# Kernel tuning notes

Hardware: AMD Instinct MI355X
Metric: run time of the kernel (lower is better)

The kernel has to match this reference:

```python
import jax, jax.numpy as jnp
import numpy as np
import math

B, T, D = 2, 2048, 1024
H = 16
DH = D // H  # 64
ROPE_BASE = 10000.0


def _rope_tables(seq_len, d_head, dtype=jnp.float32):
    inv_freq = 1.0 / (ROPE_BASE ** (jnp.arange(0, d_head, 2, dtype=jnp.float32) / d_head))
    pos = jnp.arange(seq_len, dtype=jnp.float32)
    freqs = jnp.outer(pos, inv_freq)            # [T, DH/2]
    emb = jnp.concatenate([freqs, freqs], -1)   # [T, DH]
    return jnp.cos(emb).astype(dtype), jnp.sin(emb).astype(dtype)


def _rotate_half(x):
    half = x.shape[-1] // 2
    return jnp.concatenate([-x[..., half:], x[..., :half]], axis=-1)


def setup_inputs() -> dict:
    key = jax.random.key(0)
    k1, k2, k3 = jax.random.split(key, 3)
    x = jax.random.normal(k1, (B, T, D), dtype=jnp.float32)
    qkv_w = jax.random.normal(k2, (D, 3 * D), dtype=jnp.float32) * (1.0 / math.sqrt(D))
    out_w = jax.random.normal(k3, (D, D), dtype=jnp.float32) * (1.0 / math.sqrt(D))
    out_b = jnp.zeros((D,), dtype=jnp.float32)
    mask = jnp.tril(jnp.ones((T, T), dtype=bool))[None, None]  # causal [1,1,T,T]
    return {"x": x, "mask": mask, "qkv_w": qkv_w, "out_w": out_w, "out_b": out_b}


def reference(x, mask, qkv_w, out_w, out_b):
    Bv, Tv, Dv = x.shape
    qkv = (x @ qkv_w).reshape(Bv, Tv, 3, H, DH)
    # [B, H, T, DH]
    q = jnp.transpose(qkv[:, :, 0], (0, 2, 1, 3))
    k = jnp.transpose(qkv[:, :, 1], (0, 2, 1, 3))
    v = jnp.transpose(qkv[:, :, 2], (0, 2, 1, 3))
    cos, sin = _rope_tables(Tv, DH, x.dtype)
    cos = cos[None, None]  # [1,1,T,DH]
    sin = sin[None, None]
    q = q * cos + _rotate_half(q) * sin
    k = k * cos + _rotate_half(k) * sin
    scores = jnp.einsum('bhqd,bhkd->bhqk', q, k) / math.sqrt(DH)
    scores = jnp.where(mask, scores, -jnp.inf)
    probs = jax.nn.softmax(scores, axis=-1)  # dropout = identity in eval mode
    out = jnp.einsum('bhqk,bhkd->bhqd', probs, v)
    out = jnp.transpose(out, (0, 2, 1, 3)).reshape(Bv, Tv, Dv)
    return out @ out_w + out_b
```

## Files before the change

kernel.cpp:

```cpp
#include <hip/hip_runtime.h>
#include <math.h>

typedef __attribute__((ext_vector_type(8))) short short8;
typedef __attribute__((ext_vector_type(4))) float f32x4;

static __device__ __forceinline__ unsigned short f2bf(float f) {
  unsigned u = __builtin_bit_cast(unsigned, f);
  u += 0x7fffu + ((u >> 16) & 1u);
  return (unsigned short)(u >> 16);
}
static __device__ __forceinline__ float bf2f(unsigned short h) {
  return __builtin_bit_cast(float, ((unsigned)h) << 16);
}
static __device__ __forceinline__ unsigned pack2bf(float a, float b) {
  return (unsigned)f2bf(a) | ((unsigned)f2bf(b) << 16);
}
static __device__ __forceinline__ unsigned pack2bf_t(float a, float b) {
  return __builtin_amdgcn_perm(__builtin_bit_cast(unsigned, b),
                               __builtin_bit_cast(unsigned, a), 0x07060302u);
}

typedef __attribute__((address_space(3))) unsigned short lds_us;
typedef __attribute__((address_space(1))) const unsigned short gbl_us;

static __device__ __forceinline__ void gld_lds16(const unsigned short* g,
                                                 unsigned short* l) {
  __builtin_amdgcn_global_load_lds((gbl_us*)g, (lds_us*)l, 16, 0, 0);
}

__global__ __launch_bounds__(256) void cast_x(const float* __restrict__ x,
                                              unsigned short* __restrict__ xb) {
  int i = (blockIdx.x * 256 + threadIdx.x) * 8;
  float4 a = *(const float4*)(x + i);
  float4 b = *(const float4*)(x + i + 4);
  ushort4 u0 = {f2bf(a.x), f2bf(a.y), f2bf(a.z), f2bf(a.w)};
  ushort4 u1 = {f2bf(b.x), f2bf(b.y), f2bf(b.z), f2bf(b.w)};
  *(ushort4*)(xb + i) = u0;
  *(ushort4*)(xb + i + 4) = u1;
}

__global__ __launch_bounds__(256) void tcast(const float* __restrict__ in,
                                             unsigned short* __restrict__ out,
                                             int R, int C) {
  __shared__ unsigned short T[64][68];
  const int r0 = blockIdx.y * 64, c0 = blockIdx.x * 64;
  const int tr = threadIdx.x >> 2;
  const int tc = (threadIdx.x & 3) * 16;
#pragma unroll
  for (int j = 0; j < 4; ++j) {
    float4 v = *(const float4*)(in + (size_t)(r0 + tr) * C + c0 + tc + j * 4);
    ushort4 u = {f2bf(v.x), f2bf(v.y), f2bf(v.z), f2bf(v.w)};
    *(ushort4*)&T[tr][tc + j * 4] = u;
  }
  __syncthreads();
  const int oc = tr;
#pragma unroll
  for (int g = 0; g < 4; ++g) {
    ushort4 u;
    u.x = T[tc + g * 4 + 0][oc];
    u.y = T[tc + g * 4 + 1][oc];
    u.z = T[tc + g * 4 + 2][oc];
    u.w = T[tc + g * 4 + 3][oc];
    *(ushort4*)(out + (size_t)(c0 + oc) * R + r0 + tc + g * 4) = u;
  }
}

template <int MODE>
__global__ __launch_bounds__(256) void gemm_mfma(
    const unsigned short* __restrict__ A, const unsigned short* __restrict__ BT,
    unsigned short* __restrict__ qo, unsigned short* __restrict__ ko,
    unsigned short* __restrict__ vo, const float* __restrict__ bias,
    float* __restrict__ out) {
  __shared__ unsigned short As[4096];
  __shared__ unsigned short Bs[4096];
  const int tid = threadIdx.x;
  const int w = tid >> 6;
  const int lane = tid & 63;
  const int l15 = lane & 15;
  const int quad = lane >> 4;
  const int wm = w >> 1, wn = w & 1;
  const int m0 = blockIdx.y * 128;
  const int n0 = blockIdx.x * 128;

  f32x4 acc[4][4];
  const f32x4 zero4 = {0.f, 0.f, 0.f, 0.f};
#pragma unroll
  for (int mt = 0; mt < 4; ++mt)
#pragma unroll
    for (int nt = 0; nt < 4; ++nt) acc[mt][nt] = zero4;

  int srow[2], skch[2];
#pragma unroll
  for (int i = 0; i < 2; ++i) {
    int c = i * 256 + w * 64 + lane;
    srow[i] = c >> 2;
    skch[i] = (c & 3) ^ ((srow[i] >> 1) & 3);
  }
  const unsigned short* gA[2];
  const unsigned short* gB[2];
#pragma unroll
  for (int i = 0; i < 2; ++i) {
    gA[i] = A + (size_t)(m0 + srow[i]) * 1024 + skch[i] * 8;
    gB[i] = BT + (size_t)(n0 + srow[i]) * 1024 + skch[i] * 8;
  }
  unsigned short* lA[2];
  unsigned short* lB[2];
#pragma unroll
  for (int i = 0; i < 2; ++i) {
    int c = i * 256 + w * 64 + lane;
    lA[i] = As + c * 8;
    lB[i] = Bs + c * 8;
  }

  const int swz = (quad ^ ((l15 >> 1) & 3)) * 8;
  int aoff[4], boff[4];
#pragma unroll
  for (int t = 0; t < 4; ++t) {
    aoff[t] = (wm * 64 + t * 16 + l15) * 32 + swz;
    boff[t] = (wn * 64 + t * 16 + l15) * 32 + swz;
  }

  for (int k0 = 0; k0 < 1024; k0 += 32) {
    __syncthreads();
#pragma unroll
    for (int i = 0; i < 2; ++i) {
      gld_lds16(gA[i] + k0, lA[i]);
      gld_lds16(gB[i] + k0, lB[i]);
    }
    __syncthreads();

    short8 af[4], bf[4];
#pragma unroll
    for (int t = 0; t < 4; ++t) {
      af[t] = *(const short8*)(As + aoff[t]);
      bf[t] = *(const short8*)(Bs + boff[t]);
    }
#pragma unroll
    for (int mt = 0; mt < 4; ++mt)
#pragma unroll
      for (int nt = 0; nt < 4; ++nt)
        acc[mt][nt] =
            __builtin_amdgcn_mfma_f32_16x16x32_bf16(af[mt], bf[nt], acc[mt][nt], 0, 0, 0);
  }

  if constexpr (MODE == 0) {
    const int b = m0 >> 11;
    const int nbase = n0 + wn * 64;
    const int which = nbase >> 10;
    const int h = (nbase & 1023) >> 6;
    const int bh = b * 16 + h;
    if (which < 2) {
      unsigned short* dst = which ? ko : qo;
      const float qs = (which == 0) ? 0.1803368801111f : 1.0f;
      float inv0 = expf(-((float)l15 / 32.f) * 9.21034037198f);
      float inv1 = expf(-((float)(16 + l15) / 32.f) * 9.21034037198f);
#pragma unroll
      for (int mt = 0; mt < 4; ++mt)
#pragma unroll
        for (int r = 0; r < 4; ++r) {
          int t = (m0 + wm * 64 + mt * 16 + quad * 4 + r) & 2047;
          float s0, c0, s1, c1;
          sincosf((float)t * inv0, &s0, &c0);
          sincosf((float)t * inv1, &s1, &c1);
          float x0 = acc[mt][0][r], x1 = acc[mt][1][r];
          float x2 = acc[mt][2][r], x3 = acc[mt][3][r];
          size_t rowoff = ((size_t)bh * 2048 + t) * 64 + l15;
          dst[rowoff + 0]  = f2bf((x0 * c0 - x2 * s0) * qs);
          dst[rowoff + 16] = f2bf((x1 * c1 - x3 * s1) * qs);
          dst[rowoff + 32] = f2bf((x2 * c0 + x0 * s0) * qs);
          dst[rowoff + 48] = f2bf((x3 * c1 + x1 * s1) * qs);
        }
    } else {
#pragma unroll
      for (int mt = 0; mt < 4; ++mt) {
        int t0 = (m0 + wm * 64 + mt * 16 + quad * 4) & 2047;
#pragma unroll
        for (int nt = 0; nt < 4; ++nt) {
          int dh = nt * 16 + l15;
          ushort4 st = {f2bf(acc[mt][nt][0]), f2bf(acc[mt][nt][1]),
                        f2bf(acc[mt][nt][2]), f2bf(acc[mt][nt][3])};
          *(ushort4*)(vo + ((size_t)bh * 64 + dh) * 2048 + t0) = st;
        }
      }
    }
  } else {
    const int nbase = n0 + wn * 64;
    float bv[4];
#pragma unroll
    for (int nt = 0; nt < 4; ++nt) bv[nt] = bias[nbase + nt * 16 + l15];
#pragma unroll
    for (int mt = 0; mt < 4; ++mt)
#pragma unroll
      for (int r = 0; r < 4; ++r) {
        int m = m0 + wm * 64 + mt * 16 + quad * 4 + r;
        float* orow = out + (size_t)m * 1024 + nbase + l15;
#pragma unroll
        for (int nt = 0; nt < 4; ++nt) orow[nt * 16] = acc[mt][nt][r] + bv[nt];
      }
  }
}

__global__ __launch_bounds__(256) void attn_mfma(
    const unsigned short* __restrict__ qg, const unsigned short* __restrict__ kg,
    const unsigned short* __restrict__ vtg, unsigned short* __restrict__ og,
    unsigned short* __restrict__ OpA,
    unsigned short* __restrict__ OpB,
    float* __restrict__ Lpart) {
  __shared__ unsigned short Ks[2][4096];
  __shared__ unsigned short Vt[2][4096];
  __shared__ unsigned short Ps[4 * 16 * 64];
  const int bh = blockIdx.y;
  const int slot = blockIdx.x;
  int qb, chunk;
  if (slot < 32) {
    qb = 24 + (slot & 7);
    chunk = slot >> 3;
  } else if (slot < 56) {
    int s = slot - 32;
    qb = 16 + (s & 7);
    chunk = s >> 3;
  } else if (slot < 72) {
    int s = slot - 56;
    qb = 8 + (s & 7);
    chunk = s >> 3;
  } else {
    qb = slot - 72;
    chunk = 0;
  }
  const int n = qb >= 24 ? 4 : (qb >= 16 ? 3 : (qb >= 8 ? 2 : 1));
  const int t0 = chunk * (qb + 1) / n;
  const int t1 = (chunk + 1) * (qb + 1) / n;

  const int tid = threadIdx.x;
  const int w = tid >> 6;
  const int lane = tid & 63;
  const int l15 = lane & 15;
  const int quad = lane >> 4;

  const int gq0 = qb * 64;
  const int qw = w * 16;

  const unsigned short* qrow = qg + ((size_t)bh * 2048 + gq0 + qw + l15) * 64;
  short8 qf0 = *(const short8*)(qrow + quad * 8);
  short8 qf1 = *(const short8*)(qrow + quad * 8 + 32);

  f32x4 acc_o[4];
  const f32x4 zero4 = {0.f, 0.f, 0.f, 0.f};
#pragma unroll
  for (int nt = 0; nt < 4; ++nt) acc_o[nt] = zero4;
  float lsum = 0.f;

  const unsigned short* kbase = kg + (size_t)bh * 2048 * 64;
  const unsigned short* vtbase = vtg + (size_t)bh * 64 * 2048;
  unsigned short* pb = &Ps[w * 16 * 64];
  const int prow = l15 * 64;
  const int psw = l15 & 7;

  auto issue = [&](int kb, int buf) {
    const unsigned short* ksrc = kbase + (size_t)(kb * 64) * 64;
    const unsigned short* vsrc = vtbase + kb * 64;
#pragma unroll
    for (int i = 0; i < 2; ++i) {
      int c = (w * 2 + i) * 64 + lane;
      int row = c >> 3, d = c & 7;
      int sc = d ^ (row & 7);
      gld_lds16(ksrc + row * 64 + sc * 8, &Ks[buf][c * 8]);
      gld_lds16(vsrc + (size_t)row * 2048 + sc * 8, &Vt[buf][c * 8]);
    }
  };

  const int kc0 = (quad ^ psw) * 8;
  const int kc1 = kc0 ^ 32;

  issue(t0, 0);
  for (int kb = t0; kb < t1; ++kb) {
    const int cur = (kb - t0) & 1;
    __syncthreads();
    if (kb + 1 < t1) issue(kb + 1, cur ^ 1);

    const unsigned short* kt = Ks[cur];
    const unsigned short* vt = Vt[cur];

    f32x4 s[4];
#pragma unroll
    for (int nt = 0; nt < 4; ++nt) {
      const unsigned short* kr = kt + (nt * 16 + l15) * 64;
      short8 kf0 = *(const short8*)(kr + kc0);
      short8 kf1 = *(const short8*)(kr + kc1);
      f32x4 c = zero4;
      c = __builtin_amdgcn_mfma_f32_16x16x32_bf16(kf0, qf0, c, 0, 0, 0);
      c = __builtin_amdgcn_mfma_f32_16x16x32_bf16(kf1, qf1, c, 0, 0, 0);
      s[nt] = c;
    }

    if (kb == qb) {
#pragma unroll
      for (int nt = 0; nt < 4; ++nt) {
        int klocal = nt * 16 + quad * 4;
        int qlocal = qw + l15;
#pragma unroll
        for (int r = 0; r < 4; ++r)
          if (klocal + r > qlocal) s[nt][r] = -INFINITY;
      }
    }

#pragma unroll
    for (int nt = 0; nt < 4; ++nt) {
      float e0 = exp2f(s[nt][0]);
      float e1 = exp2f(s[nt][1]);
      float e2 = exp2f(s[nt][2]);
      float e3 = exp2f(s[nt][3]);
      lsum += (e0 + e1) + (e2 + e3);
      int base = prow + ((nt * 2 + (quad >> 1)) ^ psw) * 8 + (quad & 1) * 4;
      *(unsigned*)&pb[base] = pack2bf_t(e0, e1);
      *(unsigned*)&pb[base + 2] = pack2bf_t(e2, e3);
    }

    short8 pf0 = *(const short8*)&pb[prow + (quad ^ psw) * 8];
    short8 pf1 = *(const short8*)&pb[prow + ((4 + quad) ^ psw) * 8];

#pragma unroll
    for (int nt = 0; nt < 4; ++nt) {
      const unsigned short* vr = vt + (nt * 16 + l15) * 64;
      short8 vf0 = *(const short8*)(vr + kc0);
      short8 vf1 = *(const short8*)(vr + kc1);
      acc_o[nt] = __builtin_amdgcn_mfma_f32_16x16x32_bf16(vf0, pf0, acc_o[nt], 0, 0, 0);
      acc_o[nt] = __builtin_amdgcn_mfma_f32_16x16x32_bf16(vf1, pf1, acc_o[nt], 0, 0, 0);
    }
  }

  lsum += __shfl_xor(lsum, 16);
  lsum += __shfl_xor(lsum, 32);

  if (n == 1) {
    float inv_l = 1.0f / lsum;
    const int b = bh >> 4;
    const int h = bh & 15;
    unsigned short* orow =
        og + ((size_t)(b * 2048 + gq0 + qw + l15)) * 1024 + h * 64 + quad * 4;
#pragma unroll
    for (int nt = 0; nt < 4; ++nt) {
      *(unsigned*)(orow + nt * 16) =
          pack2bf(acc_o[nt][0] * inv_l, acc_o[nt][1] * inv_l);
      *(unsigned*)(orow + nt * 16 + 2) =
          pack2bf(acc_o[nt][2] * inv_l, acc_o[nt][3] * inv_l);
    }
  } else {
    const int pidx = (qb < 16) ? (qb - 8) * 2 + chunk
                               : (qb < 24) ? 16 + (qb - 16) * 3 + chunk
                                           : 40 + (qb - 24) * 4 + chunk;
    unsigned short* obase = (pidx < 16)
                                ? OpB + ((size_t)(bh * 16 + pidx)) * 4096
                                : OpA + ((size_t)(bh * 56 + (pidx - 16))) * 4096;
    unsigned short* orow = obase + (qw + l15) * 64 + quad * 4;
#pragma unroll
    for (int nt = 0; nt < 4; ++nt) {
      *(unsigned*)(orow + nt * 16) = pack2bf(acc_o[nt][0], acc_o[nt][1]);
      *(unsigned*)(orow + nt * 16 + 2) = pack2bf(acc_o[nt][2], acc_o[nt][3]);
    }
    if (quad == 0) Lpart[(bh * 72 + pidx) * 64 + qw + l15] = lsum;
  }
}

__global__ __launch_bounds__(256) void attn_combine(
    const unsigned short* __restrict__ OpA, const unsigned short* __restrict__ OpB,
    const float* __restrict__ Lpart, unsigned short* __restrict__ og) {
  int i = blockIdx.x * 256 + threadIdx.x;
  int dh = (i & 15) * 4;
  int q = (i >> 4) & 63;
  int idx = i >> 10;
  int bh = idx / 24;
  int qr = idx - bh * 24;
  int qb = 8 + qr;
  int count = qr < 8 ? 2 : (qr < 16 ? 3 : 4);
  int pstart = qr < 8 ? qr * 2 : (qr < 16 ? 16 + (qr - 8) * 3 : 40 + (qr - 16) * 4);
  float o0 = 0.f, o1 = 0.f, o2 = 0.f, o3 = 0.f, l = 0.f;
  for (int c = 0; c < count; ++c) {
    int pidx = pstart + c;
    const unsigned short* obase =
        (pidx < 16) ? OpB + ((size_t)(bh * 16 + pidx)) * 4096
                    : OpA + ((size_t)(bh * 56 + (pidx - 16))) * 4096;
    ushort4 a = *(const ushort4*)(obase + q * 64 + dh);
    o0 += bf2f(a.x);
    o1 += bf2f(a.y);
    o2 += bf2f(a.z);
    o3 += bf2f(a.w);
    l += Lpart[(bh * 72 + pidx) * 64 + q];
  }
  float inv = 1.0f / l;
  int bb = bh >> 4, h = bh & 15;
  int t = qb * 64 + q;
  unsigned short* orow = og + ((size_t)(bb * 2048 + t)) * 1024 + h * 64 + dh;
  *(unsigned*)(orow) = pack2bf(o0 * inv, o1 * inv);
  *(unsigned*)(orow + 2) = pack2bf(o2 * inv, o3 * inv);
}

extern "C" void kernel_launch(void* const* d_in, const int* in_sizes, int n_in,
                              void* d_out, int out_size, void* d_ws,
                              size_t ws_size, hipStream_t stream) {
  const float* x = (const float*)d_in[0];
  const float* qkv_w = (const float*)d_in[2];
  const float* out_w = (const float*)d_in[3];
  const float* out_b = (const float*)d_in[4];
  float* out = (float*)d_out;

  unsigned short* xb = (unsigned short*)d_ws;
  unsigned short* wqkvT = xb + 4194304;
  unsigned short* woT = wqkvT + 3145728;
  unsigned short* qb16 = woT + 1048576;
  unsigned short* kb16 = qb16 + 4194304;
  unsigned short* vt16 = kb16 + 4194304;
  unsigned short* ab = vt16 + 4194304;
  unsigned short* OpB = ab + 4194304;
  float* Lpart = (float*)(OpB + 4194304);
  unsigned short* OpA = xb;

  cast_x<<<2048, 256, 0, stream>>>(x, xb);
  tcast<<<dim3(48, 16), 256, 0, stream>>>(qkv_w, wqkvT, 1024, 3072);
  tcast<<<dim3(16, 16), 256, 0, stream>>>(out_w, woT, 1024, 1024);
  gemm_mfma<0><<<dim3(24, 32), 256, 0, stream>>>(xb, wqkvT, qb16, kb16, vt16,
                                                 nullptr, nullptr);
  attn_mfma<<<dim3(80, 32), 256, 0, stream>>>(qb16, kb16, vt16, ab, OpA, OpB,
                                              Lpart);
  attn_combine<<<3072, 256, 0, stream>>>(OpA, OpB, Lpart, ab);
  gemm_mfma<1><<<dim3(8, 32), 256, 0, stream>>>(ab, woT, nullptr, nullptr,
                                                nullptr, out_b, out);
}
```

Before: 217.6 us.

## Double-buffer LDS tiles in MFMA GEMM to overlap loads with compute

```diff
diff --git a/kernel.cpp b/kernel.cpp
--- a/kernel.cpp
+++ b/kernel.cpp
@@ -71,8 +71,8 @@
     unsigned short* __restrict__ qo, unsigned short* __restrict__ ko,
     unsigned short* __restrict__ vo, const float* __restrict__ bias,
     float* __restrict__ out) {
-  __shared__ unsigned short As[4096];
-  __shared__ unsigned short Bs[4096];
+  __shared__ unsigned short As[2][4096];
+  __shared__ unsigned short Bs[2][4096];
   const int tid = threadIdx.x;
   const int w = tid >> 6;
   const int lane = tid & 63;
@@ -89,27 +89,17 @@
 #pragma unroll
     for (int nt = 0; nt < 4; ++nt) acc[mt][nt] = zero4;
 
-  int srow[2], skch[2];
+  int coff[2];
+  const unsigned short* gA[2];
+  const unsigned short* gB[2];
 #pragma unroll
   for (int i = 0; i < 2; ++i) {
     int c = i * 256 + w * 64 + lane;
-    srow[i] = c >> 2;
-    skch[i] = (c & 3) ^ ((srow[i] >> 1) & 3);
-  }
-  const unsigned short* gA[2];
-  const unsigned short* gB[2];
-#pragma unroll
-  for (int i = 0; i < 2; ++i) {
-    gA[i] = A + (size_t)(m0 + srow[i]) * 1024 + skch[i] * 8;
-    gB[i] = BT + (size_t)(n0 + srow[i]) * 1024 + skch[i] * 8;
-  }
-  unsigned short* lA[2];
-  unsigned short* lB[2];
-#pragma unroll
-  for (int i = 0; i < 2; ++i) {
-    int c = i * 256 + w * 64 + lane;
-    lA[i] = As + c * 8;
-    lB[i] = Bs + c * 8;
+    int srow = c >> 2;
+    int skch = (c & 3) ^ ((srow >> 1) & 3);
+    coff[i] = c * 8;
+    gA[i] = A + (size_t)(m0 + srow) * 1024 + skch * 8;
+    gB[i] = BT + (size_t)(n0 + srow) * 1024 + skch * 8;
   }
 
   const int swz = (quad ^ ((l15 >> 1) & 3)) * 8;
@@ -120,20 +110,25 @@
     boff[t] = (wn * 64 + t * 16 + l15) * 32 + swz;
   }
 
-  for (int k0 = 0; k0 < 1024; k0 += 32) {
+  auto issue = [&](int k0, int buf) {
+#pragma unroll
+    for (int i = 0; i < 2; ++i) {
+      gld_lds16(gA[i] + k0, &As[buf][coff[i]]);
+      gld_lds16(gB[i] + k0, &Bs[buf][coff[i]]);
+    }
+  };
+
+  issue(0, 0);
+  for (int it = 0; it < 32; ++it) {
+    const int cur = it & 1;
     __syncthreads();
-#pragma unroll
-    for (int i = 0; i < 2; ++i) {
-      gld_lds16(gA[i] + k0, lA[i]);
-      gld_lds16(gB[i] + k0, lB[i]);
-    }
-    __syncthreads();
+    if (it + 1 < 32) issue((it + 1) * 32, cur ^ 1);
 
     short8 af[4], bf[4];
 #pragma unroll
     for (int t = 0; t < 4; ++t) {
-      af[t] = *(const short8*)(As + aoff[t]);
-      bf[t] = *(const short8*)(Bs + boff[t]);
+      af[t] = *(const short8*)(&As[cur][aoff[t]]);
+      bf[t] = *(const short8*)(&Bs[cur][boff[t]]);
     }
 #pragma unroll
     for (int mt = 0; mt < 4; ++mt)
```

New measurement: 217.1 us. About the same (-0.3%).
